# Optimization experiments

Hardware: AMD Instinct MI355X
Metric: run time of the kernel (lower is better)

Reference implementation:

```python
import jax, jax.numpy as jnp
import numpy as np

# Static dims (chosen so check_image_size padding is a no-op)
B, C, H, W = 4, 96, 256, 256
NUM_HEADS = 4
WIN_PARAM = 8          # number of windows per dim
SUB = 4                # sub-window pixel size
WIN_H = H // WIN_PARAM  # 32: window pixel size
WIN_W = W // WIN_PARAM
SCALE = (C // NUM_HEADS) ** -0.5


def setup_inputs() -> dict:
    key = jax.random.key(0)
    ks = jax.random.split(key, 4)
    s = 0.02
    return {
        "x": jax.random.normal(ks[0], (B, C, H, W), jnp.float32),
        "q_w": jax.random.normal(ks[1], (C, C), jnp.float32) * s,
        "q_b": jnp.zeros((C,), jnp.float32),
        "kv_w": jax.random.normal(ks[2], (2 * C, C), jnp.float32) * s,
        "kv_b": jnp.zeros((2 * C,), jnp.float32),
        "proj_w": jax.random.normal(ks[3], (C, C), jnp.float32) * s,
        "proj_b": jnp.zeros((C,), jnp.float32),
    }


def reference(x, q_w, q_b, kv_w, kv_b, proj_w, proj_b):
    nWh, nWw = H // WIN_H, W // WIN_W
    nW = nWh * nWw                      # 64 windows
    swh, sww = WIN_H // SUB, WIN_W // SUB
    sNW = swh * sww                     # 64 sub-windows per window
    N = SUB * SUB                       # 16 tokens per sub-window
    d = C // NUM_HEADS

    # B C (nWh wH) (nWw wW) -> B nW wH wW C
    wx = x.reshape(B, C, nWh, WIN_H, nWw, WIN_W).transpose(0, 2, 4, 3, 5, 1)
    wx = wx.reshape(B, nW, WIN_H, WIN_W, C)
    # B nW (swh sub)(sww sub) C -> B nW sNW N C
    sx = wx.reshape(B, nW, swh, SUB, sww, SUB, C).transpose(0, 1, 2, 4, 3, 5, 6)
    sx = sx.reshape(B, nW, sNW, N, C)
    # shuffle: B sNW nW N C
    sh = sx.transpose(0, 2, 1, 3, 4)
    pooled = sh.mean(axis=3)                     # B sNW nW C
    merged = sh.reshape(B, sNW, nW * N, C)       # B sNW (nW N) C

    q = pooled @ q_w.T + q_b                     # B sNW nW C
    kv = merged @ kv_w.T + kv_b                  # B sNW nW*N 2C
    k, v = kv[..., :C], kv[..., C:]

    q = q.reshape(B, sNW, nW, NUM_HEADS, d).transpose(0, 1, 3, 2, 4) * SCALE
    k = k.reshape(B, sNW, nW * N, NUM_HEADS, d).transpose(0, 1, 3, 2, 4)
    v = v.reshape(B, sNW, nW * N, NUM_HEADS, d).transpose(0, 1, 3, 2, 4)

    attn = jax.nn.softmax(jnp.einsum('bshqd,bshkd->bshqk', q, k), axis=-1)
    o = jnp.einsum('bshqk,bshkd->bshqd', attn, v)          # B sNW nH nW d

    # B sNW nH nW d -> B nW sNW (nH d)
    o = o.transpose(0, 3, 1, 2, 4).reshape(B, nW, sNW, C)
    o = o @ proj_w.T + proj_b

    # broadcast each sub-window result to its N tokens (repeat)
    o = jnp.broadcast_to(o[:, :, :, None, :], (B, nW, sNW, N, C))
    # B nW (swh sww)(sub sub) C -> B nW wH wW C
    o = o.reshape(B, nW, swh, sww, SUB, SUB, C).transpose(0, 1, 2, 4, 3, 5, 6)
    o = o.reshape(B, nW, WIN_H, WIN_W, C)
    # B (nWh nWw) wH wW C -> B C H W
    o = o.reshape(B, nWh, nWw, WIN_H, WIN_W, C).transpose(0, 5, 1, 3, 2, 4)
    return o.reshape(B, C, H, W)
```

## Files before the change

kernel.cpp:

```cpp
#include <hip/hip_runtime.h>
#include <hip/hip_bf16.h>
#include <stdint.h>

#define PLANE 65536
#define SCALE_F 0.20412414523193154f
#define PPART 1572864
#define PSTRIDE_F2 786432

typedef __attribute__((ext_vector_type(8))) short short8;
typedef __attribute__((ext_vector_type(4))) float f32x4;

__device__ __forceinline__ unsigned pk2(float a, float b) {
  union { __hip_bfloat162 h; unsigned u; } cv;
  cv.h = __float22bfloat162_rn(make_float2(a, b));
  return cv.u;
}

__global__ __launch_bounds__(256) void prep_kernel(
    const float* __restrict__ kvw, unsigned short* __restrict__ w_a1,
    unsigned short* __restrict__ w_b2) {
  int tid = blockIdx.x * 256 + threadIdx.x;
  int side = tid / 1536;
  int r = tid % 1536;
  int frag = r >> 6;
  int lane = r & 63;
  int tile = frag / 3, ks = frag % 3;
  int od = tile * 16 + (lane & 15);
  int c0 = ks * 32 + (lane >> 4) * 8;
  int h = od >> 5, dd = od & 31;
  unsigned out[4] = {0u, 0u, 0u, 0u};
  if (dd < 24) {
    int row = (side == 0) ? (h * 24 + dd) : (96 + h * 24 + dd);
    const float* src = kvw + row * 96 + c0;
    float4 f0 = *(const float4*)src;
    float4 f1 = *(const float4*)(src + 4);
    out[0] = pk2(f0.x, f0.y); out[1] = pk2(f0.z, f0.w);
    out[2] = pk2(f1.x, f1.y); out[3] = pk2(f1.z, f1.w);
  }
  unsigned* dst =
      (unsigned*)((side == 0) ? w_a1 : w_b2) + (frag * 64 + lane) * 4;
  dst[0] = out[0]; dst[1] = out[1]; dst[2] = out[2]; dst[3] = out[3];
}

__global__ __launch_bounds__(512) void tp_kernel(const float* __restrict__ x,
                                                 unsigned short* __restrict__ xT,
                                                 float2* __restrict__ part2) {
  __shared__ unsigned Lq[48 * 128];
  int blk = blockIdx.x;
  int h = blk & 1;
  int pr = (blk >> 1) & 3;
  int swr = (blk >> 3) & 7;
  int wh = (blk >> 6) & 7;
  int b = blk >> 9;
  int t = threadIdx.x;
  int c4l = t & 31;
  int cpg = t >> 5;
  int ka = c4l >> 3;

  int r = wh * 32 + swr * 4 + pr;
  const float* xrow =
      x + ((size_t)(b * 96) * 256 + r) * 256 + (h * 32 + c4l) * 4;

  float2 pout[3];
  #pragma unroll
  for (int j = 0; j < 3; ++j) {
    int cpair = j * 16 + cpg;
    int cg = cpair >> 2;
    const float* pA = xrow + (size_t)(2 * cpair) * PLANE;
    float4 vA = *(const float4*)pA;
    float4 vB = *(const float4*)(pA + PLANE);
    pout[j].x = (vA.x + vA.y) + (vA.z + vA.w);
    pout[j].y = (vB.x + vB.y) + (vB.z + vB.w);
    unsigned w0 = pk2(vA.x, vB.x), w1 = pk2(vA.y, vB.y);
    unsigned w2 = pk2(vA.z, vB.z), w3 = pk2(vA.w, vB.w);
    int K = ka | ((cg & 7) << 2);
    int base = cpair * 128;
    int c0 = 4 * c4l;
    Lq[base + ((c0 + 0) ^ K)] = w0;
    Lq[base + ((c0 + 1) ^ K)] = w1;
    Lq[base + ((c0 + 2) ^ K)] = w2;
    Lq[base + ((c0 + 3) ^ K)] = w3;
  }

  {
    float2* pp = part2 +
        ((size_t)(((pr * 4 + b) * 8 + swr) * 8 + wh) * 2 + h) * 1536;
    #pragma unroll
    for (int j = 0; j < 3; ++j) pp[j * 512 + t] = pout[j];
  }
  __syncthreads();

  uint4* dst = (uint4*)xT + (size_t)(b * 256 + r) * 3072;
  #pragma unroll
  for (int it = 0; it < 3; ++it) {
    int id = it * 512 + t;
    int ckl = id / 12;
    int cg = id - ckl * 12;
    int sw = ckl >> 4, pw = (ckl >> 2) & 3, wwl = ckl & 3;
    int coll = wwl * 32 + sw * 4 + pw;
    int K = wwl | ((cg & 7) << 2);
    int cx = coll ^ K;
    unsigned q0 = Lq[(cg * 4 + 0) * 128 + cx];
    unsigned q1 = Lq[(cg * 4 + 1) * 128 + cx];
    unsigned q2 = Lq[(cg * 4 + 2) * 128 + cx];
    unsigned q3 = Lq[(cg * 4 + 3) * 128 + cx];
    int colkey = sw * 32 + pw * 8 + h * 4 + wwl;
    dst[colkey * 12 + cg] = make_uint4(q0, q1, q2, q3);
  }
}

__global__ __launch_bounds__(256) void qgemm_kernel(
    const float2* __restrict__ part2, const float* __restrict__ qw,
    const float* __restrict__ qb, float* __restrict__ q_ws) {
  __shared__ float pl[64 * 97];
  int blk = blockIdx.x;
  int cog = blk & 3, wh = (blk >> 2) & 7, swr = (blk >> 5) & 7, b = blk >> 8;
  int t = threadIdx.x;

  const float2* base = part2 + (size_t)((b * 8 + swr) * 8 + wh) * 3072;
  #pragma unroll
  for (int k = 0; k < 12; ++k) {
    int h = k / 6;
    int r2 = (k % 6) * 256 + t;
    int cpair = r2 >> 5;
    int c4l = t & 31;
    int rest = h * 1536 + r2;
    float2 v0 = base[rest];
    float2 v1 = base[rest + PSTRIDE_F2];
    float2 v2 = base[rest + 2 * PSTRIDE_F2];
    float2 v3 = base[rest + 3 * PSTRIDE_F2];
    float sx = (v0.x + v1.x) + (v2.x + v3.x);
    float sy = (v0.y + v1.y) + (v2.y + v3.y);
    int sw = c4l & 7, ww = h * 4 + (c4l >> 3);
    int row = sw * 8 + ww;
    pl[row * 97 + 2 * cpair] = sx * 0.0625f;
    pl[row * 97 + 2 * cpair + 1] = sy * 0.0625f;
  }
  __syncthreads();

  int wv = t >> 6, lane = t & 63;
  float acc[6] = {0.f, 0.f, 0.f, 0.f, 0.f, 0.f};
  const float* qwr = qw + (cog * 24 + wv) * 96;
  #pragma unroll 4
  for (int c = 0; c < 96; ++c) {
    float v = pl[lane * 97 + c];
    #pragma unroll
    for (int k = 0; k < 6; ++k) acc[k] += v * qwr[k * 384 + c];
  }
  int sw = lane >> 3, ww = lane & 7;
  size_t obase =
      ((size_t)((b * 64 + swr * 8 + sw) * 64) + wh * 8 + ww) * 96;
  #pragma unroll
  for (int k = 0; k < 6; ++k) {
    int co = cog * 24 + k * 4 + wv;
    q_ws[obase + co] = (acc[k] + qb[co]) * SCALE_F;
  }
}

__global__ __launch_bounds__(512, 2) void attn_kernel(
    const unsigned short* __restrict__ xT,
    const unsigned short* __restrict__ w_a1,
    const unsigned short* __restrict__ w_b2, const float* __restrict__ kvb,
    const float* __restrict__ q_ws, float* __restrict__ o_ws) {
  extern __shared__ __align__(16) char sm[];
  char* Xs = sm;
  char* Ks = sm + 32768;
  char* Vs = sm + 59392;
  char* Ps = sm + 94208;
  float* lbuf = (float*)sm;

  int bs = blockIdx.x;
  int b = bs >> 6, s = bs & 63;
  int sh = s >> 3, sw = s & 7;
  int t = threadIdx.x;
  int w = t >> 6, lane = t & 63;
  int l15 = lane & 15, quad = lane >> 4;

  int mhA1 = w >> 2, nhA1 = w & 3;
  int mhA2 = w & 3, nhA2 = w >> 2;
  int head = w & 3, khalf = w >> 2;
  int nh = w >> 2;

  short8 wa[4][3], wb[4][3];
  #pragma unroll
  for (int i = 0; i < 4; ++i)
    #pragma unroll
    for (int k = 0; k < 3; ++k) {
      wa[i][k] = *(const short8*)(w_a1 + (((4 * mhA1 + i) * 3 + k) * 64 + lane) * 8);
      wb[i][k] = *(const short8*)(w_b2 + (((4 * nhA2 + i) * 3 + k) * 64 + lane) * 8);
    }

  short8 qf[4];
  #pragma unroll
  for (int nt = 0; nt < 4; ++nt) {
    short8 f = {0, 0, 0, 0, 0, 0, 0, 0};
    if (quad < 3) {
      const float* qp =
          q_ws + ((size_t)bs * 64 + nt * 16 + l15) * 96 + head * 24 + quad * 8;
      float4 a = *(const float4*)qp;
      float4 c = *(const float4*)(qp + 4);
      union { short8 s8; unsigned u[4]; } cv;
      cv.u[0] = pk2(a.x, a.y); cv.u[1] = pk2(a.z, a.w);
      cv.u[2] = pk2(c.x, c.y); cv.u[3] = pk2(c.z, c.w);
      f = cv.s8;
    }
    qf[nt] = f;
  }

  float bK[4][4];
  #pragma unroll
  for (int i = 0; i < 4; ++i) {
    int od0 = (4 * mhA1 + i) * 16 + quad * 4;
    #pragma unroll
    for (int r = 0; r < 4; ++r) {
      int od = od0 + r, dd = od & 31, h = od >> 5;
      bK[i][r] = (dd < 24) ? kvb[h * 24 + dd] : 0.f;
    }
  }
  float bV[4];
  #pragma unroll
  for (int i = 0; i < 4; ++i) {
    int vd = (4 * nhA2 + i) * 16 + l15, dd = vd & 31, h = vd >> 5;
    bV[i] = (dd < 24) ? kvb[96 + h * 24 + dd] : 0.f;
  }

  f32x4 zz = {0.f, 0.f, 0.f, 0.f};
  f32x4 oacc[2][2];
  #pragma unroll
  for (int m = 0; m < 2; ++m)
    #pragma unroll
    for (int n = 0; n < 2; ++n) oacc[m][n] = zz;
  float lacc[4] = {0.f, 0.f, 0.f, 0.f};

  const char* sb0 = (const char*)xT + (((size_t)(b * 256 + sh * 4) * 8 + sw) * 6144);

  int off_g[3], off_l[3];
  #pragma unroll
  for (int i = 0; i < 3; ++i) {
    int l = i * 512 + t;
    int pr = l / 384;
    int rem = l - pr * 384;
    int key = pr * 32 + rem / 12;
    int c = rem - (rem / 12) * 12;
    off_g[i] = pr * 49152 + rem * 16;
    off_l[i] = key * 256 + ((c ^ (key & 7)) << 4);
  }
  uint4 stg[3];
  #pragma unroll
  for (int i = 0; i < 3; ++i) stg[i] = *(const uint4*)(sb0 + off_g[i]);

  for (int ti = 0; ti < 8; ++ti) {
    #pragma unroll
    for (int i = 0; i < 3; ++i) *(uint4*)(Xs + off_l[i]) = stg[i];
    __syncthreads();

    {
      f32x4 acc[4][2];
      #pragma unroll
      for (int i = 0; i < 4; ++i)
        #pragma unroll
        for (int n = 0; n < 2; ++n) {
          f32x4 a; a.x = bK[i][0]; a.y = bK[i][1]; a.z = bK[i][2]; a.w = bK[i][3];
          acc[i][n] = a;
        }
      short8 bx[2][3];
      #pragma unroll
      for (int n = 0; n < 2; ++n) {
        int key = (2 * nhA1 + n) * 16 + l15;
        #pragma unroll
        for (int k = 0; k < 3; ++k)
          bx[n][k] = *(const short8*)(Xs + key * 256 +
                                      (((k * 4 + quad) ^ (key & 7)) << 4));
      }
      #pragma unroll
      for (int i = 0; i < 4; ++i)
        #pragma unroll
        for (int n = 0; n < 2; ++n)
          #pragma unroll
          for (int k = 0; k < 3; ++k)
            acc[i][n] = __builtin_amdgcn_mfma_f32_16x16x32_bf16(
                wa[i][k], bx[n][k], acc[i][n], 0, 0, 0);
      #pragma unroll
      for (int i = 0; i < 4; ++i) {
        int od0 = (4 * mhA1 + i) * 16 + quad * 4;
        int dd0 = od0 & 31;
        if (dd0 < 24) {
          int h = od0 >> 5;
          #pragma unroll
          for (int n = 0; n < 2; ++n) {
            int key = (2 * nhA1 + n) * 16 + l15;
            *(int2*)(Ks + key * 208 + (h * 24 + dd0) * 2) =
                make_int2(pk2(acc[i][n].x, acc[i][n].y),
                          pk2(acc[i][n].z, acc[i][n].w));
          }
        }
      }
    }

    {
      short8 ax[2][3];
      #pragma unroll
      for (int m = 0; m < 2; ++m) {
        int key = (2 * mhA2 + m) * 16 + l15;
        #pragma unroll
        for (int k = 0; k < 3; ++k)
          ax[m][k] = *(const short8*)(Xs + key * 256 +
                                      (((k * 4 + quad) ^ (key & 7)) << 4));
      }
      #pragma unroll
      for (int m = 0; m < 2; ++m)
        #pragma unroll
        for (int n = 0; n < 4; ++n) {
          f32x4 acc; acc.x = bV[n]; acc.y = bV[n]; acc.z = bV[n]; acc.w = bV[n];
          #pragma unroll
          for (int k = 0; k < 3; ++k)
            acc = __builtin_amdgcn_mfma_f32_16x16x32_bf16(ax[m][k], wb[n][k],
                                                          acc, 0, 0, 0);
          int vd = (4 * nhA2 + n) * 16 + l15;
          int key0 = (2 * mhA2 + m) * 16 + quad * 4;
          *(int2*)(Vs + vd * 272 + key0 * 2) =
              make_int2(pk2(acc.x, acc.y), pk2(acc.z, acc.w));
        }
    }
    __syncthreads();

    if (ti < 7) {
      const char* sb = sb0 + (size_t)(ti + 1) * 32 * 8 * 6144;
      #pragma unroll
      for (int i = 0; i < 3; ++i) stg[i] = *(const uint4*)(sb + off_g[i]);
    }

    {
      f32x4 sa[4][4];
      #pragma unroll
      for (int mt = 0; mt < 4; ++mt)
        #pragma unroll
        for (int nt = 0; nt < 4; ++nt) sa[mt][nt] = zz;
      #pragma unroll
      for (int mt = 0; mt < 4; ++mt) {
        int key = khalf * 64 + mt * 16 + l15;
        short8 ak = {0, 0, 0, 0, 0, 0, 0, 0};
        if (quad < 3)
          ak = *(const short8*)(Ks + key * 208 + head * 48 + quad * 16);
        #pragma unroll
        for (int nt = 0; nt < 4; ++nt)
          sa[mt][nt] = __builtin_amdgcn_mfma_f32_16x16x32_bf16(ak, qf[nt],
                                                               sa[mt][nt], 0, 0, 0);
      }
      #pragma unroll
      for (int mt = 0; mt < 4; ++mt) {
        int key0 = khalf * 64 + mt * 16 + quad * 4;
        #pragma unroll
        for (int nt = 0; nt < 4; ++nt) {
          float e0 = __expf(sa[mt][nt].x), e1 = __expf(sa[mt][nt].y);
          float e2 = __expf(sa[mt][nt].z), e3 = __expf(sa[mt][nt].w);
          lacc[nt] += (e0 + e1) + (e2 + e3);
          *(int2*)(Ps + head * 17408 + (nt * 16 + l15) * 272 + key0 * 2) =
              make_int2(pk2(e0, e1), pk2(e2, e3));
        }
      }
      if (ti == 7) {
        #pragma unroll
        for (int nt = 0; nt < 4; ++nt) {
          float v = lacc[nt];
          v += __shfl_xor(v, 16);
          v += __shfl_xor(v, 32);
          if (quad == 0) lbuf[(head * 2 + khalf) * 64 + nt * 16 + l15] = v;
        }
      }
    }
    __syncthreads();

    #pragma unroll
    for (int ks = 0; ks < 4; ++ks) {
      short8 av[2];
      #pragma unroll
      for (int mt = 0; mt < 2; ++mt)
        av[mt] = *(const short8*)(Vs + (head * 32 + mt * 16 + l15) * 272 +
                                  ks * 64 + quad * 16);
      #pragma unroll
      for (int n = 0; n < 2; ++n) {
        short8 bp = *(const short8*)(Ps + head * 17408 +
                                     ((2 * nh + n) * 16 + l15) * 272 +
                                     ks * 64 + quad * 16);
        #pragma unroll
        for (int mt = 0; mt < 2; ++mt)
          oacc[mt][n] = __builtin_amdgcn_mfma_f32_16x16x32_bf16(av[mt], bp,
                                                                oacc[mt][n], 0, 0, 0);
      }
    }
  }

  #pragma unroll
  for (int n = 0; n < 2; ++n) {
    int q = (2 * nh + n) * 16 + l15;
    float l = lbuf[(head * 2 + 0) * 64 + q] + lbuf[(head * 2 + 1) * 64 + q];
    float inv = 1.0f / l;
    #pragma unroll
    for (int mt = 0; mt < 2; ++mt)
      #pragma unroll
      for (int r = 0; r < 4; ++r) {
        int d = mt * 16 + quad * 4 + r;
        if (d < 24)
          o_ws[((size_t)bs * 64 + q) * 96 + head * 24 + d] = oacc[mt][n][r] * inv;
      }
  }
}

__global__ __launch_bounds__(256) void proj_kernel(const float* __restrict__ o_ws,
                                                   const float* __restrict__ pw,
                                                   const float* __restrict__ pb,
                                                   float* __restrict__ out) {
  __shared__ float ol[64 * 97];
  int blk = blockIdx.x;
  int cog = blk & 3, sh = (blk >> 2) & 7, wh = (blk >> 5) & 7, b = blk >> 8;
  int t = threadIdx.x;

  #pragma unroll
  for (int k = 0; k < 24; ++k) {
    int id = k * 256 + t;
    int pair = id / 96, c = id - pair * 96;
    int sw = pair >> 3, ww = pair & 7;
    ol[pair * 97 + c] =
        o_ws[(((size_t)(b * 64 + sh * 8 + sw)) * 64 + wh * 8 + ww) * 96 + c];
  }
  __syncthreads();

  int wv = t >> 6, lane = t & 63;
  int pair = (lane & 7) * 8 + (lane >> 3);
  float acc[6] = {0.f, 0.f, 0.f, 0.f, 0.f, 0.f};
  const float* pwr = pw + (cog * 24 + wv) * 96;
  #pragma unroll 4
  for (int c = 0; c < 96; ++c) {
    float v = ol[pair * 97 + c];
    #pragma unroll
    for (int k = 0; k < 6; ++k) acc[k] += v * pwr[k * 384 + c];
  }

  #pragma unroll
  for (int k = 0; k < 6; ++k) {
    int co = cog * 24 + k * 4 + wv;
    float val = acc[k] + pb[co];
    float4 pk = make_float4(val, val, val, val);
    size_t rowbase = ((size_t)(b * 96 + co) * 256 + wh * 32 + sh * 4) * 256;
    #pragma unroll
    for (int ph = 0; ph < 4; ++ph)
      *(float4*)(out + rowbase + ph * 256 + lane * 4) = pk;
  }
}

extern "C" void kernel_launch(void* const* d_in, const int* in_sizes, int n_in,
                              void* d_out, int out_size, void* d_ws,
                              size_t ws_size, hipStream_t stream) {
  const float* x = (const float*)d_in[0];
  const float* qw = (const float*)d_in[1];
  const float* qb = (const float*)d_in[2];
  const float* kvw = (const float*)d_in[3];
  const float* kvb = (const float*)d_in[4];
  const float* pw = (const float*)d_in[5];
  const float* pb = (const float*)d_in[6];

  float* pooled_part = (float*)d_ws;
  float* q_ws = pooled_part + 4 * PPART;
  float* o_ws = q_ws + PPART;
  unsigned short* w_a1 = (unsigned short*)(o_ws + PPART);
  unsigned short* w_b2 = w_a1 + 12288;
  unsigned short* xT = w_b2 + 12288;

  static int attn_lds = 163840;
  (void)hipFuncSetAttribute((const void*)attn_kernel,
                            hipFuncAttributeMaxDynamicSharedMemorySize,
                            attn_lds);

  hipLaunchKernelGGL(prep_kernel, dim3(12), dim3(256), 0, stream, kvw, w_a1, w_b2);
  hipLaunchKernelGGL(tp_kernel, dim3(2048), dim3(512), 0, stream, x, xT,
                     (float2*)pooled_part);
  hipLaunchKernelGGL(qgemm_kernel, dim3(1024), dim3(256), 0, stream,
                     (const float2*)pooled_part, qw, qb, q_ws);
  hipLaunchKernelGGL(attn_kernel, dim3(256), dim3(512), attn_lds, stream, xT,
                     w_a1, w_b2, kvb, q_ws, o_ws);
  hipLaunchKernelGGL(proj_kernel, dim3(1024), dim3(256), 0, stream, o_ws, pw, pb,
                     (float*)d_out);
}
```

Baseline: 305.4 us.

## Load X fragments directly from global into MFMA registers, double-buffer V in LDS

The transpose kernel now writes xT in an MFMA-fragment-friendly order so the attention kernel can load its A/B operand fragments straight from global memory into registers, prefetched one tile ahead. This removes the X staging in LDS and one __syncthreads per tile iteration. V is compacted to 24 dims per head and double-buffered across iterations, and the LDS footprint shrinks. The catch is more scattered global loads and higher register pressure from holding the prefetched fragments.

```diff
diff --git a/kernel.cpp b/kernel.cpp
--- a/kernel.cpp
+++ b/kernel.cpp
@@ -6,6 +6,7 @@
 #define SCALE_F 0.20412414523193154f
 #define PPART 1572864
 #define PSTRIDE_F2 786432
+#define TI_STRIDE 1572864
 
 typedef __attribute__((ext_vector_type(8))) short short8;
 typedef __attribute__((ext_vector_type(4))) float f32x4;
@@ -94,9 +95,11 @@
   #pragma unroll
   for (int it = 0; it < 3; ++it) {
     int id = it * 512 + t;
-    int ckl = id / 12;
-    int cg = id - ckl * 12;
-    int sw = ckl >> 4, pw = (ckl >> 2) & 3, wwl = ckl & 3;
+    int sw = id / 192;
+    int r1 = id - sw * 192;
+    int cg = r1 >> 4;
+    int r2 = r1 & 15;
+    int pw = r2 >> 2, wwl = r2 & 3;
     int coll = wwl * 32 + sw * 4 + pw;
     int K = wwl | ((cg & 7) << 2);
     int cx = coll ^ K;
@@ -104,8 +107,8 @@
     unsigned q1 = Lq[(cg * 4 + 1) * 128 + cx];
     unsigned q2 = Lq[(cg * 4 + 2) * 128 + cx];
     unsigned q3 = Lq[(cg * 4 + 3) * 128 + cx];
-    int colkey = sw * 32 + pw * 8 + h * 4 + wwl;
-    dst[colkey * 12 + cg] = make_uint4(q0, q1, q2, q3);
+    int k32 = pw * 8 + h * 4 + wwl;
+    dst[sw * 384 + cg * 32 + k32] = make_uint4(q0, q1, q2, q3);
   }
 }
 
@@ -163,11 +166,11 @@
     const unsigned short* __restrict__ w_b2, const float* __restrict__ kvb,
     const float* __restrict__ q_ws, float* __restrict__ o_ws) {
   extern __shared__ __align__(16) char sm[];
-  char* Xs = sm;
-  char* Ks = sm + 32768;
-  char* Vs = sm + 59392;
-  char* Ps = sm + 94208;
-  float* lbuf = (float*)sm;
+  char* Ks = sm;
+  char* Vs0 = sm + 26624;
+  char* Vs1 = sm + 52736;
+  char* Ps = sm + 78848;
+  float* lbuf = (float*)(sm + 148480);
 
   int bs = blockIdx.x;
   int b = bs >> 6, s = bs & 63;
@@ -234,25 +237,29 @@
 
   const char* sb0 = (const char*)xT + (((size_t)(b * 256 + sh * 4) * 8 + sw) * 6144);
 
-  int off_g[3], off_l[3];
-  #pragma unroll
-  for (int i = 0; i < 3; ++i) {
-    int l = i * 512 + t;
-    int pr = l / 384;
-    int rem = l - pr * 384;
-    int key = pr * 32 + rem / 12;
-    int c = rem - (rem / 12) * 12;
-    off_g[i] = pr * 49152 + rem * 16;
-    off_l[i] = key * 256 + ((c ^ (key & 7)) << 4);
-  }
-  uint4 stg[3];
-  #pragma unroll
-  for (int i = 0; i < 3; ++i) stg[i] = *(const uint4*)(sb0 + off_g[i]);
+  int fo[3][2];
+  #pragma unroll
+  for (int k = 0; k < 3; ++k)
+    #pragma unroll
+    for (int hf = 0; hf < 2; ++hf)
+      fo[k][hf] = (((k * 4 + quad) * 32) + hf * 16 + l15) * 16;
+  int rowA1 = nhA1 * 49152;
+  int rowA2 = mhA2 * 49152;
+
+  short8 bxp[2][3], axp[2][3];
+  #pragma unroll
+  for (int n = 0; n < 2; ++n)
+    #pragma unroll
+    for (int k = 0; k < 3; ++k)
+      bxp[n][k] = *(const short8*)(sb0 + rowA1 + fo[k][n]);
+  #pragma unroll
+  for (int m = 0; m < 2; ++m)
+    #pragma unroll
+    for (int k = 0; k < 3; ++k)
+      axp[m][k] = *(const short8*)(sb0 + rowA2 + fo[k][m]);
 
   for (int ti = 0; ti < 8; ++ti) {
-    #pragma unroll
-    for (int i = 0; i < 3; ++i) *(uint4*)(Xs + off_l[i]) = stg[i];
-    __syncthreads();
+    char* Vsb = (ti & 1) ? Vs1 : Vs0;
 
     {
       f32x4 acc[4][2];
@@ -263,15 +270,6 @@
           f32x4 a; a.x = bK[i][0]; a.y = bK[i][1]; a.z = bK[i][2]; a.w = bK[i][3];
           acc[i][n] = a;
         }
-      short8 bx[2][3];
-      #pragma unroll
-      for (int n = 0; n < 2; ++n) {
-        int key = (2 * nhA1 + n) * 16 + l15;
-        #pragma unroll
-        for (int k = 0; k < 3; ++k)
-          bx[n][k] = *(const short8*)(Xs + key * 256 +
-                                      (((k * 4 + quad) ^ (key & 7)) << 4));
-      }
       #pragma unroll
       for (int i = 0; i < 4; ++i)
         #pragma unroll
@@ -279,7 +277,7 @@
           #pragma unroll
           for (int k = 0; k < 3; ++k)
             acc[i][n] = __builtin_amdgcn_mfma_f32_16x16x32_bf16(
-                wa[i][k], bx[n][k], acc[i][n], 0, 0, 0);
+                wa[i][k], bxp[n][k], acc[i][n], 0, 0, 0);
       #pragma unroll
       for (int i = 0; i < 4; ++i) {
         int od0 = (4 * mhA1 + i) * 16 + quad * 4;
@@ -298,15 +296,6 @@
     }
 
     {
-      short8 ax[2][3];
-      #pragma unroll
-      for (int m = 0; m < 2; ++m) {
-        int key = (2 * mhA2 + m) * 16 + l15;
-        #pragma unroll
-        for (int k = 0; k < 3; ++k)
-          ax[m][k] = *(const short8*)(Xs + key * 256 +
-                                      (((k * 4 + quad) ^ (key & 7)) << 4));
-      }
       #pragma unroll
       for (int m = 0; m < 2; ++m)
         #pragma unroll
@@ -314,20 +303,31 @@
           f32x4 acc; acc.x = bV[n]; acc.y = bV[n]; acc.z = bV[n]; acc.w = bV[n];
           #pragma unroll
           for (int k = 0; k < 3; ++k)
-            acc = __builtin_amdgcn_mfma_f32_16x16x32_bf16(ax[m][k], wb[n][k],
+            acc = __builtin_amdgcn_mfma_f32_16x16x32_bf16(axp[m][k], wb[n][k],
                                                           acc, 0, 0, 0);
           int vd = (4 * nhA2 + n) * 16 + l15;
-          int key0 = (2 * mhA2 + m) * 16 + quad * 4;
-          *(int2*)(Vs + vd * 272 + key0 * 2) =
-              make_int2(pk2(acc.x, acc.y), pk2(acc.z, acc.w));
+          int dd = vd & 31, hh = vd >> 5;
+          if (dd < 24) {
+            int key0 = (2 * mhA2 + m) * 16 + quad * 4;
+            *(int2*)(Vsb + (hh * 24 + dd) * 272 + key0 * 2) =
+                make_int2(pk2(acc.x, acc.y), pk2(acc.z, acc.w));
+          }
         }
     }
     __syncthreads();
 
     if (ti < 7) {
-      const char* sb = sb0 + (size_t)(ti + 1) * 32 * 8 * 6144;
-      #pragma unroll
-      for (int i = 0; i < 3; ++i) stg[i] = *(const uint4*)(sb + off_g[i]);
+      const char* sbt = sb0 + (size_t)(ti + 1) * TI_STRIDE;
+      #pragma unroll
+      for (int n = 0; n < 2; ++n)
+        #pragma unroll
+        for (int k = 0; k < 3; ++k)
+          bxp[n][k] = *(const short8*)(sbt + rowA1 + fo[k][n]);
+      #pragma unroll
+      for (int m = 0; m < 2; ++m)
+        #pragma unroll
+        for (int k = 0; k < 3; ++k)
+          axp[m][k] = *(const short8*)(sbt + rowA2 + fo[k][m]);
     }
 
     {
@@ -375,9 +375,11 @@
     for (int ks = 0; ks < 4; ++ks) {
       short8 av[2];
       #pragma unroll
-      for (int mt = 0; mt < 2; ++mt)
-        av[mt] = *(const short8*)(Vs + (head * 32 + mt * 16 + l15) * 272 +
-                                  ks * 64 + quad * 16);
+      for (int mt = 0; mt < 2; ++mt) {
+        int dloc = mt * 16 + l15;
+        int prow = head * 24 + (dloc < 24 ? dloc : 0);
+        av[mt] = *(const short8*)(Vsb + prow * 272 + ks * 64 + quad * 16);
+      }
       #pragma unroll
       for (int n = 0; n < 2; ++n) {
         short8 bp = *(const short8*)(Ps + head * 17408 +
@@ -467,7 +469,7 @@
   unsigned short* w_b2 = w_a1 + 12288;
   unsigned short* xT = w_b2 + 12288;
 
-  static int attn_lds = 163840;
+  static int attn_lds = 150528;
   (void)hipFuncSetAttribute((const void*)attn_kernel,
                             hipFuncAttributeMaxDynamicSharedMemorySize,
                             attn_lds);
```

Result: slower. 320.3 us (+4.9%).
